# Kernel tuning notes

Measured on AMD Instinct MI355X. Metric: run time of the kernel, lower is better.

Reference implementation:

```python
import jax, jax.numpy as jnp
import numpy as np
from jax import lax

B, T1, T2, C = 8, 128, 128, 256
K = 3

def setup_inputs() -> dict:
    key = jax.random.key(0)
    k1, k2, kw, kb = jax.random.split(key, 4)
    x1 = jax.random.normal(k1, (B, T1, C), dtype=jnp.float32)
    x2 = jax.random.normal(k2, (B, T2, C), dtype=jnp.float32)
    # conv2d: in_channels = 2C, out_channels = C, kernel 3x3 (OIHW)
    fan_in = 2 * C * K * K
    bound = 1.0 / np.sqrt(fan_in)
    W = jax.random.uniform(kw, (C, 2 * C, K, K), jnp.float32, -bound, bound)
    b = jax.random.uniform(kb, (C,), jnp.float32, -bound, bound)
    alpha = jnp.float32(0.5)
    return {"x1": x1, "x2": x2, "W": W, "b": b, "alpha": alpha}


def reference(x1, x2, W, b, alpha):
    # x1: [B, T1, C], x2: [B, T2, C]
    a = jnp.transpose(x1, (0, 2, 1))  # [B, C, T1]
    c2 = jnp.transpose(x2, (0, 2, 1))  # [B, C, T2]
    Bd, Cd, T1d = a.shape
    T2d = c2.shape[-1]
    # joint outer-product tensor: [B, 2C, T1, T2]
    j1 = jnp.broadcast_to(a[:, :, :, None], (Bd, Cd, T1d, T2d))
    j2 = jnp.broadcast_to(c2[:, :, None, :], (Bd, Cd, T1d, T2d))
    joint = jnp.concatenate([j1, j2], axis=1)
    out = lax.conv_general_dilated(
        joint, W, window_strides=(1, 1), padding="SAME",
        dimension_numbers=("NCHW", "OIHW", "NCHW"))
    out = out + b[None, :, None, None]
    out = jax.nn.gelu(out, approximate=False)  # torch nn.GELU default = exact erf
    out_T1 = jnp.mean(out, axis=-1)            # [B, C, T1]
    out_T1 = jnp.transpose(out_T1, (0, 2, 1))  # [B, T1, C]
    return out_T1 * alpha + x1
```

## Files before the change

### kernel.cpp

```cpp
#include <hip/hip_runtime.h>
#include <math.h>

#define B_   8
#define T_   128
#define C_   256
#define XLDP 136
#define SLDW 37
#define LOP  5

#define OFF_WS 34816
#define OFF_S1 18944
#define OFF_BV 37888
#define OFF_LO 44032
#define SMEMB  47872

typedef unsigned short ushort;
typedef ushort ushort8v __attribute__((ext_vector_type(8)));
typedef __bf16 bf16x8  __attribute__((ext_vector_type(8)));
typedef float  f32x4   __attribute__((ext_vector_type(4)));

__device__ __forceinline__ ushort f2bf(float f) {
    unsigned u = __float_as_uint(f);
    u += 0x7fffu + ((u >> 16) & 1u);
    return (ushort)(u >> 16);
}

__device__ __forceinline__ float gelu_fast(float x) {
    float x2 = x * x;
    float y2 = x * fmaf(-0.10294234f, x2, -2.30220818f);
    float e  = __builtin_amdgcn_exp2f(y2);
    return x * __builtin_amdgcn_rcpf(1.0f + e);
}

__device__ __forceinline__ ushort8v pack8(float4 lo, float4 hi) {
    ushort8v u;
    u[0] = f2bf(lo.x); u[1] = f2bf(lo.y); u[2] = f2bf(lo.z); u[3] = f2bf(lo.w);
    u[4] = f2bf(hi.x); u[5] = f2bf(hi.y); u[6] = f2bf(hi.z); u[7] = f2bf(hi.w);
    return u;
}

__global__ __launch_bounds__(512, 4) void tc_all(
    const float* __restrict__ x1, const float* __restrict__ x2,
    const float* __restrict__ W, const float* __restrict__ bias,
    const float* __restrict__ alpha_p, float* __restrict__ out)
{
    __shared__ __align__(16) char smem[SMEMB];
    ushort* Xs = (ushort*)smem;
    ushort* Ws = (ushort*)(smem + OFF_WS);
    float*  S0 = (float*)smem;
    float*  S1 = (float*)(smem + OFF_S1);
    float*  Bv = (float*)(smem + OFF_BV);
    float*  Lo = (float*)(smem + OFF_LO);

    const int u  = threadIdx.x;
    const int b  = blockIdx.x >> 6;
    const int og = blockIdx.x & 63;
    const int l  = u & 63, w = u >> 6;
    const int r16 = l & 15, kb = l >> 4;

    const int xrow = u >> 2, xcb = (u & 3) * 32;
    const size_t xoff  = (size_t)(b * T_ + xrow) * C_ + xcb;
    const size_t wbase = (size_t)og * 4 * 4608;

    f32x4 acc[2][3] = {};
    ushort8v xbuf[2][4];
    ushort   wbuf[2][9];

    {
        int base = 36 * XLDP;
        for (int i = u; i < 12 * XLDP; i += 512) Ws[base + i] = 0;
    }

    {
        const float* xs = x1 + xoff;
        #pragma unroll
        for (int c = 0; c < 4; ++c) {
            float4 lo = *(const float4*)(xs + c * 8);
            float4 hi = *(const float4*)(xs + c * 8 + 4);
            xbuf[0][c] = pack8(lo, hi);
        }
        #pragma unroll
        for (int i = 0; i < 9; ++i) {
            int d = i * 512 + u;
            int oo = d / 1152, e = d - oo * 1152;
            wbuf[0][i] = f2bf(W[wbase + (size_t)oo * 4608 + e]);
        }
    }

    #pragma unroll
    for (int r = 0; r < 4; ++r) {
        const int cur = r & 1;
        const int s   = r >> 1;
        __syncthreads();
        #pragma unroll
        for (int c = 0; c < 4; ++c)
            *(ushort8v*)&Xs[xrow * XLDP + xcb + c * 8] = xbuf[cur][c];
        #pragma unroll
        for (int i = 0; i < 9; ++i) {
            int d  = i * 512 + u;
            int oo = d / 1152, e = d - oo * 1152;
            int kk = e / 9,    r9 = e - kk * 9;
            int rd = (s == 0) ? r9 : (r9 % 3) * 3 + (r9 / 3);
            Ws[(oo * 9 + rd) * XLDP + kk] = wbuf[cur][i];
        }
        if (r < 3) {
            const int rn = r + 1, sn = rn >> 1, pn = rn & 1;
            const float* xs = (sn ? x2 : x1) + xoff + pn * 128;
            #pragma unroll
            for (int c = 0; c < 4; ++c) {
                float4 lo = *(const float4*)(xs + c * 8);
                float4 hi = *(const float4*)(xs + c * 8 + 4);
                xbuf[cur ^ 1][c] = pack8(lo, hi);
            }
            const int soff9 = (sn * 256 + pn * 128) * 9;
            #pragma unroll
            for (int i = 0; i < 9; ++i) {
                int d = i * 512 + u;
                int oo = d / 1152, e = d - oo * 1152;
                wbuf[cur ^ 1][i] = f2bf(W[wbase + (size_t)oo * 4608 + soff9 + e]);
            }
        }
        __syncthreads();
        #pragma unroll
        for (int ks = 0; ks < 4; ++ks) {
            bf16x8 af = __builtin_bit_cast(bf16x8,
                *(const ushort8v*)&Xs[(w * 16 + r16) * XLDP + ks * 32 + kb * 8]);
            #pragma unroll
            for (int nf = 0; nf < 3; ++nf) {
                bf16x8 bfr = __builtin_bit_cast(bf16x8,
                    *(const ushort8v*)&Ws[(nf * 16 + r16) * XLDP + ks * 32 + kb * 8]);
                acc[s][nf] = __builtin_amdgcn_mfma_f32_16x16x32_bf16(af, bfr, acc[s][nf], 0, 0, 0);
            }
        }
    }
    __syncthreads();

    #pragma unroll
    for (int s = 0; s < 2; ++s) {
        float* Sb = s ? S1 : S0;
        #pragma unroll
        for (int nf = 0; nf < 3; ++nf) {
            int n = nf * 16 + r16;
            if (n < 36) {
                #pragma unroll
                for (int reg = 0; reg < 4; ++reg)
                    Sb[(w * 16 + kb * 4 + reg) * SLDW + n] = acc[s][nf][reg];
            }
        }
    }
    __syncthreads();

    const int oo = u >> 7;
    const int t  = u & 127;
    const float bo = bias[og * 4 + oo];
    float a0 = 0.f, a1 = 0.f, a2 = 0.f;
    float b0 = 0.f, b1 = 0.f, b2 = 0.f;
    #pragma unroll
    for (int sh = 0; sh < 3; ++sh) {
        int row = t + sh - 1;
        if (row >= 0 && row < T_) {
            int base = row * SLDW + oo * 9 + sh * 3;
            a0 += S0[base]; a1 += S0[base + 1]; a2 += S0[base + 2];
            b0 += S1[base]; b1 += S1[base + 1]; b2 += S1[base + 2];
        }
    }
    float A3 = bo + a0 + a1 + a2;
    float Al = bo + a1 + a2;
    float Ar = bo + a0 + a1;
    Bv[(oo * 3 + 0) * T_ + t] = b0 + b1 + b2;
    Bv[(oo * 3 + 1) * T_ + t] = b1 + b2;
    Bv[(oo * 3 + 2) * T_ + t] = b0 + b1;
    __syncthreads();

    {
        int cls = (t == 0) ? 1 : ((t == T_ - 1) ? 2 : 0);
        const float* Bs = Bv + (oo * 3 + cls) * T_;
        float s0 = 0.f, s1 = 0.f, s2 = 0.f, s3 = 0.f;
        for (int j = 0; j < T_; j += 4) {
            f32x4 v = *(const f32x4*)&Bs[j];
            s0 += gelu_fast(A3 + v[0]); s1 += gelu_fast(A3 + v[1]);
            s2 += gelu_fast(A3 + v[2]); s3 += gelu_fast(A3 + v[3]);
        }
        float sm = (s0 + s1) + (s2 + s3);
        float bl = Bs[0], br = Bs[T_ - 1];
        sm += gelu_fast(Al + bl) - gelu_fast(A3 + bl);
        sm += gelu_fast(Ar + br) - gelu_fast(A3 + br);
        Lo[t * LOP + oo] = sm;
    }
    __syncthreads();

    const float kk2 = (*alpha_p) * (1.0f / (float)T_);
    {
        int row = u >> 2, c = u & 3;
        size_t go = ((size_t)(b * T_ + row)) * C_ + og * 4 + c;
        out[go] = Lo[row * LOP + c] * kk2 + x1[go];
    }
}

extern "C" void kernel_launch(void* const* d_in, const int* in_sizes, int n_in,
                              void* d_out, int out_size, void* d_ws, size_t ws_size,
                              hipStream_t stream) {
    const float* x1    = (const float*)d_in[0];
    const float* x2    = (const float*)d_in[1];
    const float* W     = (const float*)d_in[2];
    const float* bias  = (const float*)d_in[3];
    const float* alpha = (const float*)d_in[4];
    float* out = (float*)d_out;

    tc_all<<<B_ * 64, 512, 0, stream>>>(x1, x2, W, bias, alpha, out);
}
```

Baseline: 100.4 us.

## Split fused kernel into pack, GEMM and finalize kernels with bf16 pre-packing

Splits the single fused kernel into three launches. The first converts W and the inputs to bf16 once, in a layout with contiguous K for weights. The second runs the MFMA GEMM with vectorized loads into a global scratch buffer. The third does the shift-sum, GELU mean and residual per output channel. This removes redundant per-batch weight conversion and scalar strided gathers, but adds launch overhead and a round trip of the intermediate through global memory.

```diff
diff --git a/kernel.cpp b/kernel.cpp
--- a/kernel.cpp
+++ b/kernel.cpp
@@ -5,14 +5,6 @@
 #define T_   128
 #define C_   256
 #define XLDP 136
-#define SLDW 37
-#define LOP  5
-
-#define OFF_WS 34816
-#define OFF_S1 18944
-#define OFF_BV 37888
-#define OFF_LO 44032
-#define SMEMB  47872
 
 typedef unsigned short ushort;
 typedef ushort ushort8v __attribute__((ext_vector_type(8)));
@@ -32,94 +24,94 @@
     return x * __builtin_amdgcn_rcpf(1.0f + e);
 }
 
-__device__ __forceinline__ ushort8v pack8(float4 lo, float4 hi) {
-    ushort8v u;
-    u[0] = f2bf(lo.x); u[1] = f2bf(lo.y); u[2] = f2bf(lo.z); u[3] = f2bf(lo.w);
-    u[4] = f2bf(hi.x); u[5] = f2bf(hi.y); u[6] = f2bf(hi.z); u[7] = f2bf(hi.w);
-    return u;
-}
-
-__global__ __launch_bounds__(512, 4) void tc_all(
+__global__ __launch_bounds__(256) void tc_pack(
     const float* __restrict__ x1, const float* __restrict__ x2,
-    const float* __restrict__ W, const float* __restrict__ bias,
-    const float* __restrict__ alpha_p, float* __restrict__ out)
+    const float* __restrict__ W, ushort* __restrict__ Xp,
+    ushort* __restrict__ Wt)
 {
-    __shared__ __align__(16) char smem[SMEMB];
-    ushort* Xs = (ushort*)smem;
-    ushort* Ws = (ushort*)(smem + OFF_WS);
-    float*  S0 = (float*)smem;
-    float*  S1 = (float*)(smem + OFF_S1);
-    float*  Bv = (float*)(smem + OFF_BV);
-    float*  Lo = (float*)(smem + OFF_LO);
-
-    const int u  = threadIdx.x;
-    const int b  = blockIdx.x >> 6;
-    const int og = blockIdx.x & 63;
-    const int l  = u & 63, w = u >> 6;
+    const int bid = blockIdx.x, t = threadIdx.x;
+    if (bid < 256) {
+        __shared__ ushort lw[4608];
+        const float* src = W + (size_t)bid * 4608;
+        #pragma unroll
+        for (int i = 0; i < 18; ++i)
+            lw[t + i * 256] = f2bf(src[t + i * 256]);
+        __syncthreads();
+        #pragma unroll
+        for (int i = 0; i < 18; ++i) {
+            int d = t + i * 256;
+            int c = d & 255;
+            int row18 = d >> 8;
+            int s = (row18 >= 9) ? 1 : 0;
+            int r = row18 - s * 9;
+            int rsrc = (s == 0) ? r : (r % 3) * 3 + (r / 3);
+            Wt[(((size_t)s * 64 + (bid >> 2)) * 48 + (bid & 3) * 9 + r) * 256 + c]
+                = lw[(s * 256 + c) * 9 + rsrc];
+        }
+    } else {
+        int g = (bid - 256) * 256 + t;
+        int e = g * 8;
+        int s  = e >> 18;
+        int me = e & 262143;
+        const float* src = (s ? x2 : x1) + me;
+        float4 lo = *(const float4*)src;
+        float4 hi = *(const float4*)(src + 4);
+        ushort8v u;
+        u[0] = f2bf(lo.x); u[1] = f2bf(lo.y); u[2] = f2bf(lo.z); u[3] = f2bf(lo.w);
+        u[4] = f2bf(hi.x); u[5] = f2bf(hi.y); u[6] = f2bf(hi.z); u[7] = f2bf(hi.w);
+        *(ushort8v*)&Xp[e] = u;
+    }
+}
+
+__global__ __launch_bounds__(256, 4) void tc_gemm(
+    const ushort* __restrict__ Xp, const ushort* __restrict__ Wt,
+    float* __restrict__ Sg)
+{
+    __shared__ ushort Xs[64 * XLDP];
+    __shared__ ushort Ws[48 * XLDP];
+
+    const int og = blockIdx.x;
+    const int mh = blockIdx.y;
+    const int tid = threadIdx.x;
+    const int l = tid & 63, w = tid >> 6;
     const int r16 = l & 15, kb = l >> 4;
 
-    const int xrow = u >> 2, xcb = (u & 3) * 32;
-    const size_t xoff  = (size_t)(b * T_ + xrow) * C_ + xcb;
-    const size_t wbase = (size_t)og * 4 * 4608;
-
+    ushort8v xb[2][4], wb[2][3];
     f32x4 acc[2][3] = {};
-    ushort8v xbuf[2][4];
-    ushort   wbuf[2][9];
-
-    {
-        int base = 36 * XLDP;
-        for (int i = u; i < 12 * XLDP; i += 512) Ws[base + i] = 0;
-    }
-
-    {
-        const float* xs = x1 + xoff;
-        #pragma unroll
-        for (int c = 0; c < 4; ++c) {
-            float4 lo = *(const float4*)(xs + c * 8);
-            float4 hi = *(const float4*)(xs + c * 8 + 4);
-            xbuf[0][c] = pack8(lo, hi);
-        }
-        #pragma unroll
-        for (int i = 0; i < 9; ++i) {
-            int d = i * 512 + u;
-            int oo = d / 1152, e = d - oo * 1152;
-            wbuf[0][i] = f2bf(W[wbase + (size_t)oo * 4608 + e]);
-        }
-    }
+
+    auto loadr = [&](int r, int buf) {
+        int s = r >> 1, p = r & 1;
+        const ushort* xsrc = Xp + ((size_t)s * 1024 + mh * 64) * 256 + p * 128;
+        #pragma unroll
+        for (int j = 0; j < 4; ++j) {
+            int c = tid + j * 256;
+            xb[buf][j] = *(const ushort8v*)(xsrc + (size_t)(c >> 4) * 256 + (c & 15) * 8);
+        }
+        const ushort* wsrc = Wt + ((size_t)s * 64 + og) * 48 * 256 + p * 128;
+        #pragma unroll
+        for (int j = 0; j < 3; ++j) {
+            int c = tid + j * 256;
+            wb[buf][j] = *(const ushort8v*)(wsrc + (size_t)(c >> 4) * 256 + (c & 15) * 8);
+        }
+    };
+
+    loadr(0, 0);
 
     #pragma unroll
     for (int r = 0; r < 4; ++r) {
-        const int cur = r & 1;
-        const int s   = r >> 1;
+        const int cur = r & 1, s = r >> 1;
         __syncthreads();
         #pragma unroll
-        for (int c = 0; c < 4; ++c)
-            *(ushort8v*)&Xs[xrow * XLDP + xcb + c * 8] = xbuf[cur][c];
-        #pragma unroll
-        for (int i = 0; i < 9; ++i) {
-            int d  = i * 512 + u;
-            int oo = d / 1152, e = d - oo * 1152;
-            int kk = e / 9,    r9 = e - kk * 9;
-            int rd = (s == 0) ? r9 : (r9 % 3) * 3 + (r9 / 3);
-            Ws[(oo * 9 + rd) * XLDP + kk] = wbuf[cur][i];
-        }
-        if (r < 3) {
-            const int rn = r + 1, sn = rn >> 1, pn = rn & 1;
-            const float* xs = (sn ? x2 : x1) + xoff + pn * 128;
-            #pragma unroll
-            for (int c = 0; c < 4; ++c) {
-                float4 lo = *(const float4*)(xs + c * 8);
-                float4 hi = *(const float4*)(xs + c * 8 + 4);
-                xbuf[cur ^ 1][c] = pack8(lo, hi);
-            }
-            const int soff9 = (sn * 256 + pn * 128) * 9;
-            #pragma unroll
-            for (int i = 0; i < 9; ++i) {
-                int d = i * 512 + u;
-                int oo = d / 1152, e = d - oo * 1152;
-                wbuf[cur ^ 1][i] = f2bf(W[wbase + (size_t)oo * 4608 + soff9 + e]);
-            }
-        }
+        for (int j = 0; j < 4; ++j) {
+            int c = tid + j * 256;
+            *(ushort8v*)&Xs[(c >> 4) * XLDP + (c & 15) * 8] = xb[cur][j];
+        }
+        #pragma unroll
+        for (int j = 0; j < 3; ++j) {
+            int c = tid + j * 256;
+            *(ushort8v*)&Ws[(c >> 4) * XLDP + (c & 15) * 8] = wb[cur][j];
+        }
+        if (r < 3) loadr(r + 1, cur ^ 1);
         __syncthreads();
         #pragma unroll
         for (int ks = 0; ks < 4; ++ks) {
@@ -133,68 +125,70 @@
             }
         }
     }
-    __syncthreads();
 
     #pragma unroll
-    for (int s = 0; s < 2; ++s) {
-        float* Sb = s ? S1 : S0;
+    for (int s = 0; s < 2; ++s)
         #pragma unroll
         for (int nf = 0; nf < 3; ++nf) {
             int n = nf * 16 + r16;
-            if (n < 36) {
-                #pragma unroll
-                for (int reg = 0; reg < 4; ++reg)
-                    Sb[(w * 16 + kb * 4 + reg) * SLDW + n] = acc[s][nf][reg];
-            }
-        }
-    }
-    __syncthreads();
-
-    const int oo = u >> 7;
-    const int t  = u & 127;
-    const float bo = bias[og * 4 + oo];
+            if (n < 36)
+                *(f32x4*)&Sg[((size_t)(s * 64 + og) * 36 + n) * 1024
+                             + mh * 64 + w * 16 + kb * 4] = acc[s][nf];
+        }
+}
+
+__global__ __launch_bounds__(128) void tc_fin(
+    const float* __restrict__ Sg, const float* __restrict__ x1,
+    const float* __restrict__ bias, const float* __restrict__ alpha_p,
+    float* __restrict__ out)
+{
+    const int o = blockIdx.x & 255;
+    const int b = blockIdx.x >> 8;
+    const int t = threadIdx.x;
+    const int og = o >> 2, oo = o & 3;
+
+    __shared__ float Bv[3][T_];
+
+    const float* S0 = Sg + ((size_t)og * 36 + oo * 9) * 1024 + b * 128;
+    const float* S1 = Sg + ((size_t)(64 + og) * 36 + oo * 9) * 1024 + b * 128;
+
     float a0 = 0.f, a1 = 0.f, a2 = 0.f;
     float b0 = 0.f, b1 = 0.f, b2 = 0.f;
     #pragma unroll
     for (int sh = 0; sh < 3; ++sh) {
         int row = t + sh - 1;
         if (row >= 0 && row < T_) {
-            int base = row * SLDW + oo * 9 + sh * 3;
-            a0 += S0[base]; a1 += S0[base + 1]; a2 += S0[base + 2];
-            b0 += S1[base]; b1 += S1[base + 1]; b2 += S1[base + 2];
-        }
-    }
+            const float* p0 = S0 + sh * 3 * 1024 + row;
+            a0 += p0[0]; a1 += p0[1024]; a2 += p0[2048];
+            const float* p1 = S1 + sh * 3 * 1024 + row;
+            b0 += p1[0]; b1 += p1[1024]; b2 += p1[2048];
+        }
+    }
+    const float bo = bias[o];
     float A3 = bo + a0 + a1 + a2;
     float Al = bo + a1 + a2;
     float Ar = bo + a0 + a1;
-    Bv[(oo * 3 + 0) * T_ + t] = b0 + b1 + b2;
-    Bv[(oo * 3 + 1) * T_ + t] = b1 + b2;
-    Bv[(oo * 3 + 2) * T_ + t] = b0 + b1;
+    Bv[0][t] = b0 + b1 + b2;
+    Bv[1][t] = b1 + b2;
+    Bv[2][t] = b0 + b1;
     __syncthreads();
 
-    {
-        int cls = (t == 0) ? 1 : ((t == T_ - 1) ? 2 : 0);
-        const float* Bs = Bv + (oo * 3 + cls) * T_;
-        float s0 = 0.f, s1 = 0.f, s2 = 0.f, s3 = 0.f;
-        for (int j = 0; j < T_; j += 4) {
-            f32x4 v = *(const f32x4*)&Bs[j];
-            s0 += gelu_fast(A3 + v[0]); s1 += gelu_fast(A3 + v[1]);
-            s2 += gelu_fast(A3 + v[2]); s3 += gelu_fast(A3 + v[3]);
-        }
-        float sm = (s0 + s1) + (s2 + s3);
-        float bl = Bs[0], br = Bs[T_ - 1];
-        sm += gelu_fast(Al + bl) - gelu_fast(A3 + bl);
-        sm += gelu_fast(Ar + br) - gelu_fast(A3 + br);
-        Lo[t * LOP + oo] = sm;
-    }
-    __syncthreads();
+    int cls = (t == 0) ? 1 : ((t == T_ - 1) ? 2 : 0);
+    const float* Bs = Bv[cls];
+    float s0 = 0.f, s1 = 0.f, s2 = 0.f, s3 = 0.f;
+    for (int j = 0; j < T_; j += 4) {
+        f32x4 v = *(const f32x4*)&Bs[j];
+        s0 += gelu_fast(A3 + v[0]); s1 += gelu_fast(A3 + v[1]);
+        s2 += gelu_fast(A3 + v[2]); s3 += gelu_fast(A3 + v[3]);
+    }
+    float sm = (s0 + s1) + (s2 + s3);
+    float bl = Bs[0], br = Bs[T_ - 1];
+    sm += gelu_fast(Al + bl) - gelu_fast(A3 + bl);
+    sm += gelu_fast(Ar + br) - gelu_fast(A3 + br);
 
     const float kk2 = (*alpha_p) * (1.0f / (float)T_);
-    {
-        int row = u >> 2, c = u & 3;
-        size_t go = ((size_t)(b * T_ + row)) * C_ + og * 4 + c;
-        out[go] = Lo[row * LOP + c] * kk2 + x1[go];
-    }
+    size_t go = ((size_t)(b * T_ + t)) * C_ + o;
+    out[go] = sm * kk2 + x1[go];
 }
 
 extern "C" void kernel_launch(void* const* d_in, const int* in_sizes, int n_in,
@@ -207,5 +201,11 @@
     const float* alpha = (const float*)d_in[4];
     float* out = (float*)d_out;
 
-    tc_all<<<B_ * 64, 512, 0, stream>>>(x1, x2, W, bias, alpha, out);
-}
+    float*  Sg = (float*)d_ws;
+    ushort* Xp = (ushort*)((char*)d_ws + (size_t)2 * 64 * 36 * 1024 * 4);
+    ushort* Wt = Xp + (size_t)2 * 1024 * 256;
+
+    tc_pack<<<512, 256, 0, stream>>>(x1, x2, W, Xp, Wt);
+    tc_gemm<<<dim3(64, 16), 256, 0, stream>>>(Xp, Wt, Sg);
+    tc_fin<<<B_ * C_, T_, 0, stream>>>(Sg, x1, bias, alpha, out);
+}
```

Result: faster. 94.81 us (-5.6%).
